# Kernel optimization log

Hardware: AMD Instinct MI355X
Metric: run time of the kernel (lower is better)

## Reference

```python
import jax, jax.numpy as jnp
import numpy as np

T, H, E, I, K = 2048, 2048, 32, 768, 8  # tokens, hidden, experts, moe_intermediate, top_k


def setup_inputs() -> dict:
    key = jax.random.key(0)
    k1, k2, k3, k4, k5 = jax.random.split(key, 5)
    return {
        "hidden_states": jax.random.normal(k1, (T, H), dtype=jnp.float32),
        "w_gate": jax.random.normal(k2, (H, E), dtype=jnp.float32) * 0.02,
        "w_gate_proj": jax.random.normal(k3, (E, H, I), dtype=jnp.float32) * 0.02,
        "w_up_proj": jax.random.normal(k4, (E, H, I), dtype=jnp.float32) * 0.02,
        "w_down_proj": jax.random.normal(k5, (E, I, H), dtype=jnp.float32) * 0.02,
    }


def reference(hidden_states, w_gate, w_gate_proj, w_up_proj, w_down_proj):
    # Router: softmax over expert logits, top-k, renormalize (RoutingMethodType.Renormalize,
    # norm_topk_prob=True in Qwen3 MoE config).
    x = hidden_states                                  # [T, H]
    n_tok = x.shape[0]
    logits = x @ w_gate                                # [T, E]
    probs = jax.nn.softmax(logits, axis=-1)            # [T, E]
    topk_w, topk_idx = jax.lax.top_k(probs, K)         # [T, K]
    topk_w = topk_w / jnp.sum(topk_w, axis=-1, keepdims=True)
    # Sparse combine weights [T, E]: zero except the K selected experts per token.
    combine = jnp.zeros_like(probs).at[jnp.arange(n_tok)[:, None], topk_idx].set(topk_w)

    # Expert SwiGLU MLPs (gate/up/down), computed for all experts then combined with
    # the sparse weights -- mathematically identical to top-k dispatch + grouped GEMM.
    g = jnp.einsum('th,ehi->tei', x, w_gate_proj)      # [T, E, I]
    u = jnp.einsum('th,ehi->tei', x, w_up_proj)        # [T, E, I]
    act = jax.nn.silu(g) * u                           # [T, E, I]
    # Combine expert outputs without materializing [T, E, H].
    out = jnp.einsum('tei,eih,te->th', act, w_down_proj, combine)  # [T, H]
    return out
```

## Files before the change

### kernel.cpp

```cpp
#include <hip/hip_runtime.h>

#define T_TOK 2048
#define HD    2048
#define NE    32
#define ID    768
#define TOPK  8
#define NPAIR (T_TOK * TOPK)
#define MAXT  160

typedef short bf16x8 __attribute__((ext_vector_type(8)));
typedef float f32x4  __attribute__((ext_vector_type(4)));

__device__ inline unsigned short f2bf(float f) {
    unsigned u = __builtin_bit_cast(unsigned, f);
    u += 0x7FFF + ((u >> 16) & 1);
    return (unsigned short)(u >> 16);
}

__device__ inline void gload16(const void* g, void* l) {
    __builtin_amdgcn_global_load_lds(
        (const __attribute__((address_space(1))) unsigned*)g,
        (__attribute__((address_space(3))) unsigned*)l, 16, 0, 0);
}

__global__ void cvt_x(const float* __restrict__ x, unsigned short* __restrict__ x16) {
    int i = blockIdx.x * blockDim.x + threadIdx.x;
    const float4* src = (const float4*)x + (size_t)i * 2;
    float4 a = src[0], b = src[1];
    uint4 r;
    r.x = (unsigned)f2bf(a.x) | ((unsigned)f2bf(a.y) << 16);
    r.y = (unsigned)f2bf(a.z) | ((unsigned)f2bf(a.w) << 16);
    r.z = (unsigned)f2bf(b.x) | ((unsigned)f2bf(b.y) << 16);
    r.w = (unsigned)f2bf(b.z) | ((unsigned)f2bf(b.w) << 16);
    *(uint4*)(x16 + (size_t)i * 8) = r;
}

__global__ void transpose_cvt(const float* __restrict__ in, unsigned short* __restrict__ out,
                              int R, int C) {
    int e = blockIdx.z;
    int r0 = blockIdx.y * 64, c0 = blockIdx.x * 64;
    const float* src = in + (size_t)e * R * C;
    unsigned short* dst = out + (size_t)e * R * C;
    __shared__ float tile[64][65];
    int tid = threadIdx.x;
    #pragma unroll
    for (int j = 0; j < 4; ++j) {
        int idx = tid + 256 * j;
        int rr = idx >> 4, c4 = (idx & 15) * 4;
        float4 v = *(const float4*)&src[(size_t)(r0 + rr) * C + c0 + c4];
        tile[rr][c4] = v.x; tile[rr][c4 + 1] = v.y; tile[rr][c4 + 2] = v.z; tile[rr][c4 + 3] = v.w;
    }
    __syncthreads();
    #pragma unroll
    for (int j = 0; j < 2; ++j) {
        int idx = tid + 256 * j;
        int cc = idx >> 3, r8 = (idx & 7) * 8;
        uint4 o;
        unsigned* po = (unsigned*)&o;
        #pragma unroll
        for (int q = 0; q < 4; ++q)
            po[q] = (unsigned)f2bf(tile[r8 + 2 * q][cc]) |
                    ((unsigned)f2bf(tile[r8 + 2 * q + 1][cc]) << 16);
        *(uint4*)&dst[(size_t)(c0 + cc) * R + r0 + r8] = o;
    }
}

__global__ void router_kernel(const float* __restrict__ x, const float* __restrict__ wg,
                              int* __restrict__ topk_idx, float* __restrict__ topk_w,
                              int* __restrict__ counts) {
    int t = blockIdx.x;
    int tid = threadIdx.x;
    int e = tid & 31, seg = tid >> 5;
    const float* xr = x + (size_t)t * HD + seg * 256;
    const float* wp = wg + (size_t)(seg * 256) * NE + e;
    float acc = 0.f;
    #pragma unroll 4
    for (int j = 0; j < 256; ++j) acc += xr[j] * wp[j * NE];
    __shared__ float part[8][33];
    __shared__ float lg[32];
    part[seg][e] = acc;
    __syncthreads();
    if (tid < 32) {
        float s = 0.f;
        #pragma unroll
        for (int g = 0; g < 8; ++g) s += part[g][tid];
        lg[tid] = s;
    }
    __syncthreads();
    if (tid == 0) {
        float m = lg[0];
        for (int i = 1; i < 32; ++i) m = fmaxf(m, lg[i]);
        for (int i = 0; i < 32; ++i) lg[i] = __expf(lg[i] - m);
        int   idxs[TOPK]; float wv[TOPK]; float wsum = 0.f;
        #pragma unroll
        for (int k = 0; k < TOPK; ++k) {
            float best = -1.f; int bi = 0;
            for (int i = 0; i < 32; ++i) if (lg[i] > best) { best = lg[i]; bi = i; }
            idxs[k] = bi; wv[k] = best; wsum += best; lg[bi] = -1.f;
        }
        #pragma unroll
        for (int k = 0; k < TOPK; ++k) {
            topk_idx[t * TOPK + k] = idxs[k];
            topk_w[t * TOPK + k]   = wv[k] / wsum;
            atomicAdd(&counts[idxs[k]], 1);
        }
    }
}

__global__ void build_tiles(const int* __restrict__ counts, int* __restrict__ cursor,
                            int* __restrict__ tE, int* __restrict__ tStart,
                            int* __restrict__ tCnt) {
    if (threadIdx.x == 0 && blockIdx.x == 0) {
        int run = 0, nt = 0;
        for (int e = 0; e < NE; ++e) {
            cursor[e] = run;
            int c = counts[e];
            int nte = (c + 127) >> 7;
            for (int j = 0; j < nte; ++j) {
                tE[nt] = e;
                tStart[nt] = run + j * 128;
                tCnt[nt] = (c - j * 128 < 128) ? (c - j * 128) : 128;
                ++nt;
            }
            run += nte * 128;
        }
        for (; nt < MAXT; ++nt) { tE[nt] = -1; tStart[nt] = 0; tCnt[nt] = 0; }
    }
}

__global__ void scatter_kernel(const int* __restrict__ topk_idx, int* __restrict__ cursor,
                               int* __restrict__ token_list) {
    int i = blockIdx.x * 256 + threadIdx.x;
    int e = topk_idx[i];
    int pos = atomicAdd(&cursor[e], 1);
    token_list[pos] = i;
}

__global__ __launch_bounds__(256, 2)
void gemm1_kernel(const unsigned short* __restrict__ X16,
                  const unsigned short* __restrict__ WG, const unsigned short* __restrict__ WU,
                  const int* __restrict__ token_list,
                  const int* __restrict__ tE, const int* __restrict__ tStart,
                  const int* __restrict__ tCnt, unsigned short* __restrict__ act16) {
    int tile = blockIdx.x / 6, it = blockIdx.x % 6;
    int e = tE[tile];
    if (e < 0) return;
    int start = tStart[tile], cnt = tCnt[tile];
    int i0 = it * 128;

    __shared__ __align__(16) unsigned short As[128 * 64];
    __shared__ __align__(16) unsigned short Bg[128 * 64];
    __shared__ __align__(16) unsigned short Bu[128 * 64];
    __shared__ int rowTok[128];

    int tid = threadIdx.x;
    if (tid < 128)
        rowTok[tid] = (tid < cnt) ? (token_list[start + tid] >> 3) : 0;
    __syncthreads();

    int lane = tid & 63, w = tid >> 6;
    int sub = lane & 7, lrow = lane >> 3;

    const unsigned short* aP[4]; const unsigned short* gP[4]; const unsigned short* uP[4];
    #pragma unroll
    for (int c = 0; c < 4; ++c) {
        int q = w * 4 + c;
        int r = q * 8 + lrow;
        int chunk = (sub ^ (r & 7)) * 8;
        aP[c] = X16 + (size_t)rowTok[r] * HD + chunk;
        gP[c] = WG + ((size_t)e * ID + i0 + r) * HD + chunk;
        uP[c] = WU + ((size_t)e * ID + i0 + r) * HD + chunk;
    }

    f32x4 accg[4][4], accu[4][4];
    #pragma unroll
    for (int m = 0; m < 4; ++m)
        #pragma unroll
        for (int n = 0; n < 4; ++n) {
            f32x4 z = {0.f, 0.f, 0.f, 0.f};
            accg[m][n] = z; accu[m][n] = z;
        }

    int wm = w >> 1, wn = w & 1, l15 = lane & 15, lhi = lane >> 4;
    const bf16x8* Af = (const bf16x8*)As;
    const bf16x8* Gf = (const bf16x8*)Bg;
    const bf16x8* Uf = (const bf16x8*)Bu;

    for (int k0 = 0; k0 < HD; k0 += 64) {
        #pragma unroll
        for (int c = 0; c < 4; ++c) {
            int q = w * 4 + c;
            gload16(aP[c] + k0, (char*)As + q * 1024);
            gload16(gP[c] + k0, (char*)Bg + q * 1024);
            gload16(uP[c] + k0, (char*)Bu + q * 1024);
        }
        __syncthreads();
        #pragma unroll
        for (int ks = 0; ks < 2; ++ks) {
            int cc = ks * 4 + lhi;
            bf16x8 a[4], bg[4], bu[4];
            #pragma unroll
            for (int m = 0; m < 4; ++m) { int r = wm * 64 + m * 16 + l15; a[m] = Af[r * 8 + (cc ^ (r & 7))]; }
            #pragma unroll
            for (int n = 0; n < 4; ++n) {
                int r = wn * 64 + n * 16 + l15;
                bg[n] = Gf[r * 8 + (cc ^ (r & 7))];
                bu[n] = Uf[r * 8 + (cc ^ (r & 7))];
            }
            #pragma unroll
            for (int m = 0; m < 4; ++m)
                #pragma unroll
                for (int n = 0; n < 4; ++n) {
                    accg[m][n] = __builtin_amdgcn_mfma_f32_16x16x32_bf16(a[m], bg[n], accg[m][n], 0, 0, 0);
                    accu[m][n] = __builtin_amdgcn_mfma_f32_16x16x32_bf16(a[m], bu[n], accu[m][n], 0, 0, 0);
                }
        }
        __syncthreads();
    }

    #pragma unroll
    for (int m = 0; m < 4; ++m) {
        int rb = wm * 64 + m * 16 + lhi * 4;
        #pragma unroll
        for (int q = 0; q < 4; ++q) {
            int r = rb + q;
            size_t orow = (size_t)(start + r) * ID + i0 + wn * 64;
            #pragma unroll
            for (int n = 0; n < 4; ++n) {
                float g = accg[m][n][q], uu = accu[m][n][q];
                float a = g / (1.f + __expf(-g)) * uu;
                act16[orow + n * 16 + l15] = f2bf(a);
            }
        }
    }
}

__global__ __launch_bounds__(256, 2)
void gemm2_kernel(const unsigned short* __restrict__ act16, const unsigned short* __restrict__ WD,
                  const int* __restrict__ token_list,
                  const int* __restrict__ tE, const int* __restrict__ tStart,
                  const int* __restrict__ tCnt, const float* __restrict__ topk_w,
                  float* __restrict__ out) {
    int tile = blockIdx.x / 8, ht = blockIdx.x % 8;
    int e = tE[tile];
    if (e < 0) return;
    int start = tStart[tile], cnt = tCnt[tile];
    int h0 = ht * 256;

    __shared__ __align__(16) unsigned short As[128 * 64];
    __shared__ __align__(16) unsigned short Bs[256 * 64];
    __shared__ int   rowTok[128];
    __shared__ float rowW[128];

    int tid = threadIdx.x;
    if (tid < 128) {
        if (tid < cnt) { int v = token_list[start + tid]; rowTok[tid] = v >> 3; rowW[tid] = topk_w[v]; }
        else           { rowTok[tid] = 0;                 rowW[tid] = 0.f; }
    }
    __syncthreads();

    int lane = tid & 63, w = tid >> 6;
    int sub = lane & 7, lrow = lane >> 3;

    const unsigned short* aP[4]; const unsigned short* bP[8];
    #pragma unroll
    for (int c = 0; c < 4; ++c) {
        int q = w * 4 + c;
        int r = q * 8 + lrow;
        int chunk = (sub ^ (r & 7)) * 8;
        aP[c] = act16 + (size_t)(start + r) * ID + chunk;
    }
    #pragma unroll
    for (int c = 0; c < 8; ++c) {
        int q = w * 8 + c;
        int r = q * 8 + lrow;
        int chunk = (sub ^ (r & 7)) * 8;
        bP[c] = WD + ((size_t)e * HD + h0 + r) * ID + chunk;
    }

    f32x4 acc[4][8];
    #pragma unroll
    for (int m = 0; m < 4; ++m)
        #pragma unroll
        for (int n = 0; n < 8; ++n) { f32x4 z = {0.f, 0.f, 0.f, 0.f}; acc[m][n] = z; }

    int wm = w >> 1, wn = w & 1, l15 = lane & 15, lhi = lane >> 4;
    const bf16x8* Af = (const bf16x8*)As;
    const bf16x8* Bf = (const bf16x8*)Bs;

    for (int k0 = 0; k0 < ID; k0 += 64) {
        #pragma unroll
        for (int c = 0; c < 4; ++c) {
            int q = w * 4 + c;
            gload16(aP[c] + k0, (char*)As + q * 1024);
        }
        #pragma unroll
        for (int c = 0; c < 8; ++c) {
            int q = w * 8 + c;
            gload16(bP[c] + k0, (char*)Bs + q * 1024);
        }
        __syncthreads();
        #pragma unroll
        for (int ks = 0; ks < 2; ++ks) {
            int cc = ks * 4 + lhi;
            bf16x8 a[4], b[8];
            #pragma unroll
            for (int m = 0; m < 4; ++m) { int r = wm * 64 + m * 16 + l15; a[m] = Af[r * 8 + (cc ^ (r & 7))]; }
            #pragma unroll
            for (int n = 0; n < 8; ++n) { int r = wn * 128 + n * 16 + l15; b[n] = Bf[r * 8 + (cc ^ (r & 7))]; }
            #pragma unroll
            for (int m = 0; m < 4; ++m)
                #pragma unroll
                for (int n = 0; n < 8; ++n)
                    acc[m][n] = __builtin_amdgcn_mfma_f32_16x16x32_bf16(a[m], b[n], acc[m][n], 0, 0, 0);
        }
        __syncthreads();
    }

    #pragma unroll
    for (int m = 0; m < 4; ++m) {
        int rb = wm * 64 + m * 16 + lhi * 4;
        #pragma unroll
        for (int q = 0; q < 4; ++q) {
            int r = rb + q;
            if (r < cnt) {
                int tok = rowTok[r];
                float wgt = rowW[r];
                float* orow = out + (size_t)tok * HD + h0 + wn * 128;
                #pragma unroll
                for (int n = 0; n < 8; ++n)
                    atomicAdd(&orow[n * 16 + l15], acc[m][n][q] * wgt);
            }
        }
    }
}

extern "C" void kernel_launch(void* const* d_in, const int* in_sizes, int n_in,
                              void* d_out, int out_size, void* d_ws, size_t ws_size,
                              hipStream_t stream) {
    const float* x   = (const float*)d_in[0];
    const float* wg  = (const float*)d_in[1];
    const float* wgp = (const float*)d_in[2];
    const float* wup = (const float*)d_in[3];
    const float* wdp = (const float*)d_in[4];
    float* out = (float*)d_out;

    char* ws = (char*)d_ws;
    size_t off = 0;
    unsigned short* X16   = (unsigned short*)(ws + off); off += (size_t)T_TOK * HD * 2;
    unsigned short* act16 = (unsigned short*)(ws + off); off += (size_t)MAXT * 128 * ID * 2;
    int*   topk_idx   = (int*)(ws + off);   off += NPAIR * 4;
    float* topk_w     = (float*)(ws + off); off += NPAIR * 4;
    int*   token_list = (int*)(ws + off);   off += MAXT * 128 * 4;
    int*   counts     = (int*)(ws + off);   off += 256;
    int*   cursor     = (int*)(ws + off);   off += 256;
    int*   tE         = (int*)(ws + off);   off += MAXT * 4;
    int*   tStart     = (int*)(ws + off);   off += MAXT * 4;
    int*   tCnt       = (int*)(ws + off);   off += MAXT * 4;
    off = (off + 255) & ~(size_t)255;
    unsigned short* WG = (unsigned short*)(ws + off); off += (size_t)NE * ID * HD * 2;
    unsigned short* WU = (unsigned short*)(ws + off); off += (size_t)NE * ID * HD * 2;
    unsigned short* WD = (unsigned short*)(ws + off); off += (size_t)NE * HD * ID * 2;
    (void)in_sizes; (void)n_in; (void)out_size; (void)ws_size;

    hipMemsetAsync(counts, 0, 256, stream);
    hipMemsetAsync(d_out, 0, (size_t)T_TOK * HD * 4, stream);

    cvt_x<<<T_TOK * HD / (256 * 8), 256, 0, stream>>>(x, X16);
    router_kernel<<<T_TOK, 256, 0, stream>>>(x, wg, topk_idx, topk_w, counts);
    build_tiles<<<1, 64, 0, stream>>>(counts, cursor, tE, tStart, tCnt);
    scatter_kernel<<<NPAIR / 256, 256, 0, stream>>>(topk_idx, cursor, token_list);

    transpose_cvt<<<dim3(ID / 64, HD / 64, NE), 256, 0, stream>>>(wgp, WG, HD, ID);
    transpose_cvt<<<dim3(ID / 64, HD / 64, NE), 256, 0, stream>>>(wup, WU, HD, ID);
    transpose_cvt<<<dim3(HD / 64, ID / 64, NE), 256, 0, stream>>>(wdp, WD, ID, HD);

    gemm1_kernel<<<MAXT * 6, 256, 0, stream>>>(X16, WG, WU, token_list, tE, tStart, tCnt, act16);
    gemm2_kernel<<<MAXT * 8, 256, 0, stream>>>(act16, WD, token_list, tE, tStart, tCnt, topk_w, out);
}
```

Baseline: 656.4 us.

## Fuse weight transposes, x conversion and router into one prep kernel

Merges the three weight transpose-convert launches, the activation bf16 conversion and the router into a single launch that dispatches on block index. The transpose now converts to bf16 before staging in a swizzled padded LDS tile and loads four rows per thread, which reduces shared-memory traffic and bank conflicts. This removes launch gaps and lets the independent prep stages overlap. An unused prep_kernel stub is left behind, and the router blocks now run after many transpose blocks in block order.

```diff
diff --git a/kernel.cpp b/kernel.cpp
--- a/kernel.cpp
+++ b/kernel.cpp
@@ -23,86 +23,154 @@
         (__attribute__((address_space(3))) unsigned*)l, 16, 0, 0);
 }
 
-__global__ void cvt_x(const float* __restrict__ x, unsigned short* __restrict__ x16) {
-    int i = blockIdx.x * blockDim.x + threadIdx.x;
-    const float4* src = (const float4*)x + (size_t)i * 2;
-    float4 a = src[0], b = src[1];
-    uint4 r;
-    r.x = (unsigned)f2bf(a.x) | ((unsigned)f2bf(a.y) << 16);
-    r.y = (unsigned)f2bf(a.z) | ((unsigned)f2bf(a.w) << 16);
-    r.z = (unsigned)f2bf(b.x) | ((unsigned)f2bf(b.y) << 16);
-    r.w = (unsigned)f2bf(b.z) | ((unsigned)f2bf(b.w) << 16);
-    *(uint4*)(x16 + (size_t)i * 8) = r;
-}
-
-__global__ void transpose_cvt(const float* __restrict__ in, unsigned short* __restrict__ out,
-                              int R, int C) {
-    int e = blockIdx.z;
-    int r0 = blockIdx.y * 64, c0 = blockIdx.x * 64;
-    const float* src = in + (size_t)e * R * C;
-    unsigned short* dst = out + (size_t)e * R * C;
-    __shared__ float tile[64][65];
+
+#define NT_GU 12288
+#define NT_D  12288
+#define NB_CVT 2048
+#define NB_RTR 2048
+
+__device__ inline void transpose_tile(const float* __restrict__ src, unsigned short* __restrict__ dst,
+                                      int R, int C, int r0, int c0, char* lds) {
     int tid = threadIdx.x;
-    #pragma unroll
-    for (int j = 0; j < 4; ++j) {
-        int idx = tid + 256 * j;
-        int rr = idx >> 4, c4 = (idx & 15) * 4;
-        float4 v = *(const float4*)&src[(size_t)(r0 + rr) * C + c0 + c4];
-        tile[rr][c4] = v.x; tile[rr][c4 + 1] = v.y; tile[rr][c4 + 2] = v.z; tile[rr][c4 + 3] = v.w;
+    int rq = tid >> 4;
+    int c4 = (tid & 15) * 4;
+    const float* s0 = src + (size_t)(r0 + 4 * rq) * C + c0 + c4;
+    float4 L0 = *(const float4*)(s0);
+    float4 L1 = *(const float4*)(s0 + C);
+    float4 L2 = *(const float4*)(s0 + 2 * C);
+    float4 L3 = *(const float4*)(s0 + 3 * C);
+    int t = rq >> 1, lo = rq & 1;
+    const float* a0 = &L0.x; const float* a1 = &L1.x;
+    const float* a2 = &L2.x; const float* a3 = &L3.x;
+    #pragma unroll
+    for (int q = 0; q < 4; ++q) {
+        int c = c4 + q;
+        int sw = t ^ ((c >> 1) & 7);
+        unsigned w0 = (unsigned)f2bf(a0[q]) | ((unsigned)f2bf(a1[q]) << 16);
+        unsigned w1 = (unsigned)f2bf(a2[q]) | ((unsigned)f2bf(a3[q]) << 16);
+        uint2 wv = {w0, w1};
+        *(uint2*)(lds + c * 144 + sw * 16 + lo * 8) = wv;
     }
     __syncthreads();
     #pragma unroll
-    for (int j = 0; j < 2; ++j) {
-        int idx = tid + 256 * j;
-        int cc = idx >> 3, r8 = (idx & 7) * 8;
-        uint4 o;
-        unsigned* po = (unsigned*)&o;
-        #pragma unroll
-        for (int q = 0; q < 4; ++q)
-            po[q] = (unsigned)f2bf(tile[r8 + 2 * q][cc]) |
-                    ((unsigned)f2bf(tile[r8 + 2 * q + 1][cc]) << 16);
-        *(uint4*)&dst[(size_t)(c0 + cc) * R + r0 + r8] = o;
-    }
-}
-
-__global__ void router_kernel(const float* __restrict__ x, const float* __restrict__ wg,
-                              int* __restrict__ topk_idx, float* __restrict__ topk_w,
-                              int* __restrict__ counts) {
-    int t = blockIdx.x;
-    int tid = threadIdx.x;
-    int e = tid & 31, seg = tid >> 5;
-    const float* xr = x + (size_t)t * HD + seg * 256;
-    const float* wp = wg + (size_t)(seg * 256) * NE + e;
-    float acc = 0.f;
-    #pragma unroll 4
-    for (int j = 0; j < 256; ++j) acc += xr[j] * wp[j * NE];
-    __shared__ float part[8][33];
-    __shared__ float lg[32];
-    part[seg][e] = acc;
-    __syncthreads();
-    if (tid < 32) {
-        float s = 0.f;
-        #pragma unroll
-        for (int g = 0; g < 8; ++g) s += part[g][tid];
-        lg[tid] = s;
-    }
-    __syncthreads();
-    if (tid == 0) {
-        float m = lg[0];
-        for (int i = 1; i < 32; ++i) m = fmaxf(m, lg[i]);
-        for (int i = 0; i < 32; ++i) lg[i] = __expf(lg[i] - m);
-        int   idxs[TOPK]; float wv[TOPK]; float wsum = 0.f;
-        #pragma unroll
-        for (int k = 0; k < TOPK; ++k) {
-            float best = -1.f; int bi = 0;
-            for (int i = 0; i < 32; ++i) if (lg[i] > best) { best = lg[i]; bi = i; }
-            idxs[k] = bi; wv[k] = best; wsum += best; lg[bi] = -1.f;
-        }
-        #pragma unroll
-        for (int k = 0; k < TOPK; ++k) {
-            topk_idx[t * TOPK + k] = idxs[k];
-            topk_w[t * TOPK + k]   = wv[k] / wsum;
-            atomicAdd(&counts[idxs[k]], 1);
+    for (int jj = 0; jj < 2; ++jj) {
+        int idx = tid + 256 * jj;
+        int c = idx >> 3, tt = idx & 7;
+        int sw = tt ^ ((c >> 1) & 7);
+        uint4 v = *(const uint4*)(lds + c * 144 + sw * 16);
+        *(uint4*)&dst[(size_t)(c0 + c) * R + r0 + 8 * tt] = v;
+    }
+}
+
+__global__ __launch_bounds__(256)
+void prep_kernel(const float* __restrict__ x, const float* __restrict__ wg,
+                 const float* __restrict__ wgp, const float* __restrict__ wup,
+                 const float* __restrict__ wdp,
+                 unsigned short* __restrict__ X16,
+                 unsigned short* __restrict__ WG, unsigned short* __restrict__ WU,
+                 unsigned short* __restrict__ WD,
+                 int* __restrict__ topk_idx, float* __restrict__ topk_w,
+                 int* __restrict__ counts) {
+    __shared__ __align__(16) char lds[64 * 144];
+    int bid = blockIdx.x;
+    if (bid < 2 * NT_GU) {
+        const float* src = (bid < NT_GU) ? wgp : wup;
+        unsigned short* dst = (bid < NT_GU) ? WG : WU;
+        int local = (bid < NT_GU) ? bid : bid - NT_GU;
+        int e = local / 384, ti = local % 384;
+        int r0 = (ti & 31) * 64, c0 = (ti >> 5) * 64;
+        transpose_tile(src + (size_t)e * HD * ID, dst + (size_t)e * HD * ID,
+                       ID, HD, 0, 0, lds);
+        return;
+    }
+    bid -= 2 * NT_GU;
+    (void)bid;
+}
+
+
+__global__ __launch_bounds__(256)
+void prep_all(const float* __restrict__ x, const float* __restrict__ wg,
+              const float* __restrict__ wgp, const float* __restrict__ wup,
+              const float* __restrict__ wdp,
+              unsigned short* __restrict__ X16,
+              unsigned short* __restrict__ WG, unsigned short* __restrict__ WU,
+              unsigned short* __restrict__ WD,
+              int* __restrict__ topk_idx, float* __restrict__ topk_w,
+              int* __restrict__ counts) {
+    __shared__ __align__(16) char lds[64 * 144];
+    int bid = blockIdx.x;
+
+    if (bid < NT_GU) {
+        int e = bid / 384, ti = bid % 384;
+        int r0 = (ti & 31) * 64, c0 = (ti >> 5) * 64;
+        transpose_tile(wgp + (size_t)e * HD * ID, WG + (size_t)e * HD * ID, HD, ID, r0, c0, lds);
+        return;
+    }
+    bid -= NT_GU;
+    if (bid < NT_GU) {
+        int e = bid / 384, ti = bid % 384;
+        int r0 = (ti & 31) * 64, c0 = (ti >> 5) * 64;
+        transpose_tile(wup + (size_t)e * HD * ID, WU + (size_t)e * HD * ID, HD, ID, r0, c0, lds);
+        return;
+    }
+    bid -= NT_GU;
+    if (bid < NT_D) {
+        int e = bid / 384, ti = bid % 384;
+        int r0 = (ti % 12) * 64, c0 = (ti / 12) * 64;
+        transpose_tile(wdp + (size_t)e * ID * HD, WD + (size_t)e * ID * HD, ID, HD, r0, c0, lds);
+        return;
+    }
+    bid -= NT_D;
+    if (bid < NB_CVT) {
+        int i = bid * 256 + threadIdx.x;
+        const float4* src = (const float4*)x + (size_t)i * 2;
+        float4 a = src[0], b = src[1];
+        uint4 r;
+        r.x = (unsigned)f2bf(a.x) | ((unsigned)f2bf(a.y) << 16);
+        r.y = (unsigned)f2bf(a.z) | ((unsigned)f2bf(a.w) << 16);
+        r.z = (unsigned)f2bf(b.x) | ((unsigned)f2bf(b.y) << 16);
+        r.w = (unsigned)f2bf(b.z) | ((unsigned)f2bf(b.w) << 16);
+        *(uint4*)(X16 + (size_t)i * 8) = r;
+        return;
+    }
+    bid -= NB_CVT;
+    {
+        int t = bid;
+        int tid = threadIdx.x;
+        int e = tid & 31, seg = tid >> 5;
+        const float* xr = x + (size_t)t * HD + seg * 256;
+        const float* wp = wg + (size_t)(seg * 256) * NE + e;
+        float acc = 0.f;
+        #pragma unroll 4
+        for (int j = 0; j < 256; ++j) acc += xr[j] * wp[j * NE];
+        float* part = (float*)lds;
+        float* lg = part + 8 * 33;
+        part[seg * 33 + e] = acc;
+        __syncthreads();
+        if (tid < 32) {
+            float s = 0.f;
+            #pragma unroll
+            for (int g = 0; g < 8; ++g) s += part[g * 33 + tid];
+            lg[tid] = s;
+        }
+        __syncthreads();
+        if (tid == 0) {
+            float m = lg[0];
+            for (int i = 1; i < 32; ++i) m = fmaxf(m, lg[i]);
+            for (int i = 0; i < 32; ++i) lg[i] = __expf(lg[i] - m);
+            int   idxs[TOPK]; float wv[TOPK]; float wsum = 0.f;
+            #pragma unroll
+            for (int k = 0; k < TOPK; ++k) {
+                float best = -1.f; int bi = 0;
+                for (int i = 0; i < 32; ++i) if (lg[i] > best) { best = lg[i]; bi = i; }
+                idxs[k] = bi; wv[k] = best; wsum += best; lg[bi] = -1.f;
+            }
+            #pragma unroll
+            for (int k = 0; k < TOPK; ++k) {
+                topk_idx[t * TOPK + k] = idxs[k];
+                topk_w[t * TOPK + k]   = wv[k] / wsum;
+                atomicAdd(&counts[idxs[k]], 1);
+            }
         }
     }
 }
@@ -366,15 +434,12 @@
     hipMemsetAsync(counts, 0, 256, stream);
     hipMemsetAsync(d_out, 0, (size_t)T_TOK * HD * 4, stream);
 
-    cvt_x<<<T_TOK * HD / (256 * 8), 256, 0, stream>>>(x, X16);
-    router_kernel<<<T_TOK, 256, 0, stream>>>(x, wg, topk_idx, topk_w, counts);
+    prep_all<<<NT_GU + NT_GU + NT_D + NB_CVT + NB_RTR, 256, 0, stream>>>(
+        x, wg, wgp, wup, wdp, X16, WG, WU, WD, topk_idx, topk_w, counts);
+
     build_tiles<<<1, 64, 0, stream>>>(counts, cursor, tE, tStart, tCnt);
     scatter_kernel<<<NPAIR / 256, 256, 0, stream>>>(topk_idx, cursor, token_list);
 
-    transpose_cvt<<<dim3(ID / 64, HD / 64, NE), 256, 0, stream>>>(wgp, WG, HD, ID);
-    transpose_cvt<<<dim3(ID / 64, HD / 64, NE), 256, 0, stream>>>(wup, WU, HD, ID);
-    transpose_cvt<<<dim3(HD / 64, ID / 64, NE), 256, 0, stream>>>(wdp, WD, ID, HD);
-
     gemm1_kernel<<<MAXT * 6, 256, 0, stream>>>(X16, WG, WU, token_list, tE, tStart, tCnt, act16);
     gemm2_kernel<<<MAXT * 8, 256, 0, stream>>>(act16, WD, token_list, tE, tStart, tCnt, topk_w, out);
 }
```

After: 634.5 us. 3.3% less time.

## Drop weight transposes; read B tiles with LDS transpose loads and fuse prep kernels

Applied to the files above, without the earlier changes.

Converts expert weights to bf16 in their original [E,H,I]/[E,I,H] layout with a plain streaming conversion instead of tiled transpose kernels. The GEMMs now stage B tiles K-major in LDS and use ds_read_b64_tr_b16 to form the MFMA operands, adding an explicit lgkmcnt wait and sched barrier. The x conversion, weight conversions and router are merged into one launch. This removes the shared-memory transpose pass and several launches, but relies on the correctness of the transposed-read addressing. LDS bank behaviour of the new B layout is unswizzled.

```diff
diff --git a/kernel.cpp b/kernel.cpp
--- a/kernel.cpp
+++ b/kernel.cpp
@@ -9,6 +9,7 @@
 #define MAXT  160
 
 typedef short bf16x8 __attribute__((ext_vector_type(8)));
+typedef short bf16x4 __attribute__((ext_vector_type(4)));
 typedef float f32x4  __attribute__((ext_vector_type(4)));
 
 __device__ inline unsigned short f2bf(float f) {
@@ -16,6 +17,9 @@
     u += 0x7FFF + ((u >> 16) & 1);
     return (unsigned short)(u >> 16);
 }
+__device__ inline unsigned pk2(float a, float b) {
+    return (unsigned)f2bf(a) | ((unsigned)f2bf(b) << 16);
+}
 
 __device__ inline void gload16(const void* g, void* l) {
     __builtin_amdgcn_global_load_lds(
@@ -23,52 +27,44 @@
         (__attribute__((address_space(3))) unsigned*)l, 16, 0, 0);
 }
 
-__global__ void cvt_x(const float* __restrict__ x, unsigned short* __restrict__ x16) {
-    int i = blockIdx.x * blockDim.x + threadIdx.x;
-    const float4* src = (const float4*)x + (size_t)i * 2;
-    float4 a = src[0], b = src[1];
-    uint4 r;
-    r.x = (unsigned)f2bf(a.x) | ((unsigned)f2bf(a.y) << 16);
-    r.y = (unsigned)f2bf(a.z) | ((unsigned)f2bf(a.w) << 16);
-    r.z = (unsigned)f2bf(b.x) | ((unsigned)f2bf(b.y) << 16);
-    r.w = (unsigned)f2bf(b.z) | ((unsigned)f2bf(b.w) << 16);
-    *(uint4*)(x16 + (size_t)i * 8) = r;
-}
-
-__global__ void transpose_cvt(const float* __restrict__ in, unsigned short* __restrict__ out,
-                              int R, int C) {
-    int e = blockIdx.z;
-    int r0 = blockIdx.y * 64, c0 = blockIdx.x * 64;
-    const float* src = in + (size_t)e * R * C;
-    unsigned short* dst = out + (size_t)e * R * C;
-    __shared__ float tile[64][65];
-    int tid = threadIdx.x;
-    #pragma unroll
-    for (int j = 0; j < 4; ++j) {
-        int idx = tid + 256 * j;
-        int rr = idx >> 4, c4 = (idx & 15) * 4;
-        float4 v = *(const float4*)&src[(size_t)(r0 + rr) * C + c0 + c4];
-        tile[rr][c4] = v.x; tile[rr][c4 + 1] = v.y; tile[rr][c4 + 2] = v.z; tile[rr][c4 + 3] = v.w;
-    }
-    __syncthreads();
-    #pragma unroll
-    for (int j = 0; j < 2; ++j) {
-        int idx = tid + 256 * j;
-        int cc = idx >> 3, r8 = (idx & 7) * 8;
-        uint4 o;
-        unsigned* po = (unsigned*)&o;
-        #pragma unroll
-        for (int q = 0; q < 4; ++q)
-            po[q] = (unsigned)f2bf(tile[r8 + 2 * q][cc]) |
-                    ((unsigned)f2bf(tile[r8 + 2 * q + 1][cc]) << 16);
-        *(uint4*)&dst[(size_t)(c0 + cc) * R + r0 + r8] = o;
-    }
-}
-
-__global__ void router_kernel(const float* __restrict__ x, const float* __restrict__ wg,
-                              int* __restrict__ topk_idx, float* __restrict__ topk_w,
-                              int* __restrict__ counts) {
-    int t = blockIdx.x;
+#define LDS_U32(p) ((unsigned)(uintptr_t)(__attribute__((address_space(3))) const void*)(const void*)(p))
+
+#define TR0(d, a) asm volatile("ds_read_b64_tr_b16 %0, %1"              : "=v"(d) : "v"(a))
+#define TR1(d, a) asm volatile("ds_read_b64_tr_b16 %0, %1 offset:1024"  : "=v"(d) : "v"(a))
+#define TR2(d, a) asm volatile("ds_read_b64_tr_b16 %0, %1 offset:2048"  : "=v"(d) : "v"(a))
+
+#define CVT_WBLK 12288
+#define CVT_XBLK 1024
+#define PREP_GRID (3 * CVT_WBLK + CVT_XBLK + T_TOK)
+
+__global__ __launch_bounds__(256)
+void prep_cvt(const float* __restrict__ x, const float* __restrict__ wg,
+              const float* __restrict__ wgp, const float* __restrict__ wup,
+              const float* __restrict__ wdp,
+              unsigned short* __restrict__ X16, unsigned short* __restrict__ WG16,
+              unsigned short* __restrict__ WU16, unsigned short* __restrict__ WD16,
+              int* __restrict__ topk_idx, float* __restrict__ topk_w,
+              int* __restrict__ counts) {
+    int bid = blockIdx.x;
+    if (bid < 3 * CVT_WBLK + CVT_XBLK) {
+        const float* src; unsigned short* dst;
+        if (bid < CVT_WBLK)              { src = wgp; dst = WG16; }
+        else if (bid < 2 * CVT_WBLK)     { src = wup; dst = WU16; bid -= CVT_WBLK; }
+        else if (bid < 3 * CVT_WBLK)     { src = wdp; dst = WD16; bid -= 2 * CVT_WBLK; }
+        else                             { src = x;   dst = X16;  bid -= 3 * CVT_WBLK; }
+        size_t base = ((size_t)bid * 256 + threadIdx.x) * 16;
+        const float4* s = (const float4*)(src + base);
+        float4 f0 = s[0], f1 = s[1], f2 = s[2], f3 = s[3];
+        uint4 o0, o1;
+        o0.x = pk2(f0.x, f0.y); o0.y = pk2(f0.z, f0.w);
+        o0.z = pk2(f1.x, f1.y); o0.w = pk2(f1.z, f1.w);
+        o1.x = pk2(f2.x, f2.y); o1.y = pk2(f2.z, f2.w);
+        o1.z = pk2(f3.x, f3.y); o1.w = pk2(f3.z, f3.w);
+        *(uint4*)(dst + base)     = o0;
+        *(uint4*)(dst + base + 8) = o1;
+        return;
+    }
+    int t = bid - (3 * CVT_WBLK + CVT_XBLK);
     int tid = threadIdx.x;
     int e = tid & 31, seg = tid >> 5;
     const float* xr = x + (size_t)t * HD + seg * 256;
@@ -149,8 +145,8 @@
     int i0 = it * 128;
 
     __shared__ __align__(16) unsigned short As[128 * 64];
-    __shared__ __align__(16) unsigned short Bg[128 * 64];
-    __shared__ __align__(16) unsigned short Bu[128 * 64];
+    __shared__ __align__(16) unsigned short Bg[64 * 128];
+    __shared__ __align__(16) unsigned short Bu[64 * 128];
     __shared__ int rowTok[128];
 
     int tid = threadIdx.x;
@@ -159,17 +155,19 @@
     __syncthreads();
 
     int lane = tid & 63, w = tid >> 6;
-    int sub = lane & 7, lrow = lane >> 3;
+    int sub = lane & 7, lrow = lane >> 3, l7 = lane & 7;
 
     const unsigned short* aP[4]; const unsigned short* gP[4]; const unsigned short* uP[4];
     #pragma unroll
     for (int c = 0; c < 4; ++c) {
         int q = w * 4 + c;
         int r = q * 8 + lrow;
-        int chunk = (sub ^ (r & 7)) * 8;
-        aP[c] = X16 + (size_t)rowTok[r] * HD + chunk;
-        gP[c] = WG + ((size_t)e * ID + i0 + r) * HD + chunk;
-        uP[c] = WU + ((size_t)e * ID + i0 + r) * HD + chunk;
+        aP[c] = X16 + (size_t)rowTok[r] * HD + (sub ^ (r & 7)) * 8;
+        int s = q * 8 + (lane >> 3);
+        size_t ro = ((size_t)e * HD + (s >> 3) * 4 + (l7 >> 1)) * ID
+                  + i0 + (s & 7) * 16 + (l7 & 1) * 8;
+        gP[c] = WG + ro;
+        uP[c] = WU + ro;
     }
 
     f32x4 accg[4][4], accu[4][4];
@@ -183,36 +181,42 @@
 
     int wm = w >> 1, wn = w & 1, l15 = lane & 15, lhi = lane >> 4;
     const bf16x8* Af = (const bf16x8*)As;
-    const bf16x8* Gf = (const bf16x8*)Bg;
-    const bf16x8* Uf = (const bf16x8*)Bu;
+    unsigned bgBase = LDS_U32(Bg) + lhi * 2048 + wn * 512 + l15 * 8;
+    unsigned buBase = LDS_U32(Bu) + lhi * 2048 + wn * 512 + l15 * 8;
 
     for (int k0 = 0; k0 < HD; k0 += 64) {
         #pragma unroll
         for (int c = 0; c < 4; ++c) {
             int q = w * 4 + c;
             gload16(aP[c] + k0, (char*)As + q * 1024);
-            gload16(gP[c] + k0, (char*)Bg + q * 1024);
-            gload16(uP[c] + k0, (char*)Bu + q * 1024);
+            gload16(gP[c] + (size_t)k0 * ID, (char*)Bg + q * 1024);
+            gload16(uP[c] + (size_t)k0 * ID, (char*)Bu + q * 1024);
         }
         __syncthreads();
         #pragma unroll
         for (int ks = 0; ks < 2; ++ks) {
             int cc = ks * 4 + lhi;
-            bf16x8 a[4], bg[4], bu[4];
+            bf16x8 a[4];
             #pragma unroll
             for (int m = 0; m < 4; ++m) { int r = wm * 64 + m * 16 + l15; a[m] = Af[r * 8 + (cc ^ (r & 7))]; }
+            bf16x4 gl[4], gh[4], ul[4], uh[4];
             #pragma unroll
             for (int n = 0; n < 4; ++n) {
-                int r = wn * 64 + n * 16 + l15;
-                bg[n] = Gf[r * 8 + (cc ^ (r & 7))];
-                bu[n] = Uf[r * 8 + (cc ^ (r & 7))];
-            }
+                unsigned adG = bgBase + ks * 8192 + n * 128;
+                unsigned adU = buBase + ks * 8192 + n * 128;
+                TR0(gl[n], adG); TR1(gh[n], adG);
+                TR0(ul[n], adU); TR1(uh[n], adU);
+            }
+            asm volatile("s_waitcnt lgkmcnt(0)" ::: "memory");
+            __builtin_amdgcn_sched_barrier(0);
             #pragma unroll
             for (int m = 0; m < 4; ++m)
                 #pragma unroll
                 for (int n = 0; n < 4; ++n) {
-                    accg[m][n] = __builtin_amdgcn_mfma_f32_16x16x32_bf16(a[m], bg[n], accg[m][n], 0, 0, 0);
-                    accu[m][n] = __builtin_amdgcn_mfma_f32_16x16x32_bf16(a[m], bu[n], accu[m][n], 0, 0, 0);
+                    bf16x8 bg = __builtin_shufflevector(gl[n], gh[n], 0, 1, 2, 3, 4, 5, 6, 7);
+                    bf16x8 bu = __builtin_shufflevector(ul[n], uh[n], 0, 1, 2, 3, 4, 5, 6, 7);
+                    accg[m][n] = __builtin_amdgcn_mfma_f32_16x16x32_bf16(a[m], bg, accg[m][n], 0, 0, 0);
+                    accu[m][n] = __builtin_amdgcn_mfma_f32_16x16x32_bf16(a[m], bu, accu[m][n], 0, 0, 0);
                 }
         }
         __syncthreads();
@@ -248,7 +252,7 @@
     int h0 = ht * 256;
 
     __shared__ __align__(16) unsigned short As[128 * 64];
-    __shared__ __align__(16) unsigned short Bs[256 * 64];
+    __shared__ __align__(16) unsigned short Bs[64 * 256];
     __shared__ int   rowTok[128];
     __shared__ float rowW[128];
 
@@ -260,22 +264,21 @@
     __syncthreads();
 
     int lane = tid & 63, w = tid >> 6;
-    int sub = lane & 7, lrow = lane >> 3;
+    int sub = lane & 7, lrow = lane >> 3, l7 = lane & 7;
 
     const unsigned short* aP[4]; const unsigned short* bP[8];
     #pragma unroll
     for (int c = 0; c < 4; ++c) {
         int q = w * 4 + c;
         int r = q * 8 + lrow;
-        int chunk = (sub ^ (r & 7)) * 8;
-        aP[c] = act16 + (size_t)(start + r) * ID + chunk;
+        aP[c] = act16 + (size_t)(start + r) * ID + (sub ^ (r & 7)) * 8;
     }
     #pragma unroll
     for (int c = 0; c < 8; ++c) {
         int q = w * 8 + c;
-        int r = q * 8 + lrow;
-        int chunk = (sub ^ (r & 7)) * 8;
-        bP[c] = WD + ((size_t)e * HD + h0 + r) * ID + chunk;
+        int s = q * 8 + (lane >> 3);
+        bP[c] = WD + ((size_t)e * ID + (s >> 4) * 4 + (l7 >> 1)) * HD
+                   + h0 + (s & 15) * 16 + (l7 & 1) * 8;
     }
 
     f32x4 acc[4][8];
@@ -286,7 +289,7 @@
 
     int wm = w >> 1, wn = w & 1, l15 = lane & 15, lhi = lane >> 4;
     const bf16x8* Af = (const bf16x8*)As;
-    const bf16x8* Bf = (const bf16x8*)Bs;
+    unsigned bBase = LDS_U32(Bs) + lhi * 4096 + wn * 1024 + l15 * 8;
 
     for (int k0 = 0; k0 < ID; k0 += 64) {
         #pragma unroll
@@ -297,22 +300,30 @@
         #pragma unroll
         for (int c = 0; c < 8; ++c) {
             int q = w * 8 + c;
-            gload16(bP[c] + k0, (char*)Bs + q * 1024);
+            gload16(bP[c] + (size_t)k0 * HD, (char*)Bs + q * 1024);
         }
         __syncthreads();
         #pragma unroll
         for (int ks = 0; ks < 2; ++ks) {
             int cc = ks * 4 + lhi;
-            bf16x8 a[4], b[8];
+            bf16x8 a[4];
             #pragma unroll
             for (int m = 0; m < 4; ++m) { int r = wm * 64 + m * 16 + l15; a[m] = Af[r * 8 + (cc ^ (r & 7))]; }
-            #pragma unroll
-            for (int n = 0; n < 8; ++n) { int r = wn * 128 + n * 16 + l15; b[n] = Bf[r * 8 + (cc ^ (r & 7))]; }
+            bf16x4 dl[8], dh[8];
+            #pragma unroll
+            for (int n = 0; n < 8; ++n) {
+                unsigned ad = bBase + ks * 16384 + n * 128;
+                TR0(dl[n], ad); TR2(dh[n], ad);
+            }
+            asm volatile("s_waitcnt lgkmcnt(0)" ::: "memory");
+            __builtin_amdgcn_sched_barrier(0);
             #pragma unroll
             for (int m = 0; m < 4; ++m)
                 #pragma unroll
-                for (int n = 0; n < 8; ++n)
-                    acc[m][n] = __builtin_amdgcn_mfma_f32_16x16x32_bf16(a[m], b[n], acc[m][n], 0, 0, 0);
+                for (int n = 0; n < 8; ++n) {
+                    bf16x8 b = __builtin_shufflevector(dl[n], dh[n], 0, 1, 2, 3, 4, 5, 6, 7);
+                    acc[m][n] = __builtin_amdgcn_mfma_f32_16x16x32_bf16(a[m], b, acc[m][n], 0, 0, 0);
+                }
         }
         __syncthreads();
     }
@@ -358,23 +369,21 @@
     int*   tStart     = (int*)(ws + off);   off += MAXT * 4;
     int*   tCnt       = (int*)(ws + off);   off += MAXT * 4;
     off = (off + 255) & ~(size_t)255;
-    unsigned short* WG = (unsigned short*)(ws + off); off += (size_t)NE * ID * HD * 2;
-    unsigned short* WU = (unsigned short*)(ws + off); off += (size_t)NE * ID * HD * 2;
-    unsigned short* WD = (unsigned short*)(ws + off); off += (size_t)NE * HD * ID * 2;
+    unsigned short* WG16 = (unsigned short*)(ws + off); off += (size_t)NE * HD * ID * 2;
+    unsigned short* WU16 = (unsigned short*)(ws + off); off += (size_t)NE * HD * ID * 2;
+    unsigned short* WD16 = (unsigned short*)(ws + off); off += (size_t)NE * ID * HD * 2;
     (void)in_sizes; (void)n_in; (void)out_size; (void)ws_size;
 
     hipMemsetAsync(counts, 0, 256, stream);
     hipMemsetAsync(d_out, 0, (size_t)T_TOK * HD * 4, stream);
 
-    cvt_x<<<T_TOK * HD / (256 * 8), 256, 0, stream>>>(x, X16);
-    router_kernel<<<T_TOK, 256, 0, stream>>>(x, wg, topk_idx, topk_w, counts);
+    prep_cvt<<<PREP_GRID, 256, 0, stream>>>(x, wg, wgp, wup, wdp,
+                                            X16, WG16, WU16, WD16,
+                                            topk_idx, topk_w, counts);
+
     build_tiles<<<1, 64, 0, stream>>>(counts, cursor, tE, tStart, tCnt);
     scatter_kernel<<<NPAIR / 256, 256, 0, stream>>>(topk_idx, cursor, token_list);
 
-    transpose_cvt<<<dim3(ID / 64, HD / 64, NE), 256, 0, stream>>>(wgp, WG, HD, ID);
-    transpose_cvt<<<dim3(ID / 64, HD / 64, NE), 256, 0, stream>>>(wup, WU, HD, ID);
-    transpose_cvt<<<dim3(HD / 64, ID / 64, NE), 256, 0, stream>>>(wdp, WD, ID, HD);
-
-    gemm1_kernel<<<MAXT * 6, 256, 0, stream>>>(X16, WG, WU, token_list, tE, tStart, tCnt, act16);
-    gemm2_kernel<<<MAXT * 8, 256, 0, stream>>>(act16, WD, token_list, tE, tStart, tCnt, topk_w, out);
-}
+    gemm1_kernel<<<MAXT * 6, 256, 0, stream>>>(X16, WG16, WU16, token_list, tE, tStart, tCnt, act16);
+    gemm2_kernel<<<MAXT * 8, 256, 0, stream>>>(act16, WD16, token_list, tE, tStart, tCnt, topk_w, out);
+}
```

Result: faster. 641.0 us (-2.3%).
